# Performance work log

Measured on AMD Instinct MI355X. Metric: run time of the kernel, lower is better.

Reference implementation:

```python
import jax, jax.numpy as jnp
import numpy as np
import math

B, C, L, E, N = 16, 256, 2048, 512, 64
H = 2 * C  # S4 model dimension


def setup_inputs() -> dict:
    key = jax.random.key(0)
    ks = jax.random.split(key, 12)
    inp = {
        "x": jax.random.normal(ks[0], (B, C, L), dtype=jnp.float32),
        "diffusion_emb": jax.random.normal(ks[1], (B, E), dtype=jnp.float32),
        "dp_W": jax.random.normal(ks[2], (C, E), dtype=jnp.float32) / np.sqrt(E).astype(np.float32),
        "dp_b": jnp.zeros((C,), dtype=jnp.float32),
        "in_W": jax.random.normal(ks[3], (H, C), dtype=jnp.float32) / np.sqrt(C).astype(np.float32),
        "in_b": jnp.zeros((H,), dtype=jnp.float32),
        "out_W": jax.random.normal(ks[4], (2 * C, C), dtype=jnp.float32) / np.sqrt(C).astype(np.float32),
        "out_b": jnp.zeros((2 * C,), dtype=jnp.float32),
        "ln1_g": jnp.ones((H,), dtype=jnp.float32),
        "ln1_b": jnp.zeros((H,), dtype=jnp.float32),
        "ln2_g": jnp.ones((H,), dtype=jnp.float32),
        "ln2_b": jnp.zeros((H,), dtype=jnp.float32),
    }
    for i, pre in enumerate(["s41_", "s42_"]):
        k = jax.random.fold_in(key, 100 + i)
        k1, k2, k3, k4, k5 = jax.random.split(k, 5)
        # dt log-uniform in [1e-3, 1e-1] (standard S4 init)
        inp[pre + "log_dt"] = (jax.random.uniform(k1, (H,)) * (math.log(0.1) - math.log(0.001)) + math.log(0.001)).astype(jnp.float32)
        inp[pre + "A_re"] = (-0.5 * jnp.ones((H, N))).astype(jnp.float32)
        inp[pre + "A_im"] = jnp.tile(math.pi * jnp.arange(N, dtype=jnp.float32), (H, 1))
        inp[pre + "C_re"] = jax.random.normal(k2, (H, N), dtype=jnp.float32) * (0.5 ** 0.5)
        inp[pre + "C_im"] = jax.random.normal(k3, (H, N), dtype=jnp.float32) * (0.5 ** 0.5)
        inp[pre + "D"] = jax.random.normal(k4, (H,), dtype=jnp.float32)
        inp[pre + "oW"] = jax.random.normal(k5, (2 * H, H), dtype=jnp.float32) / np.sqrt(H).astype(np.float32)
        inp[pre + "ob"] = jnp.zeros((2 * H,), dtype=jnp.float32)
    return inp


def _s4(u, log_dt, A_re, A_im, C_re, C_im, D, oW, ob):
    # u: [B, H, L]. Diagonal SSM (S4D, ZOH discretization) -> FFT conv -> D skip -> GELU -> GLU output linear.
    Lq = u.shape[-1]
    dt = jnp.exp(log_dt)                       # [H]
    A = A_re + 1j * A_im                       # [H, N] diagonal state matrix
    Cc = C_re + 1j * C_im                      # [H, N]
    dtA = dt[:, None] * A                      # [H, N]
    Ct = Cc * (jnp.exp(dtA) - 1.0) / A         # ZOH-discretized C*B (B = 1)
    lr = jnp.arange(Lq)
    # Vandermonde kernel: K[h, l] = 2 Re sum_n Ct[h, n] exp(dtA[h, n] * l)
    K = 2.0 * jnp.real(jnp.einsum("hn,hnl->hl", Ct, jnp.exp(dtA[:, :, None] * lr)))  # [H, L]
    nfft = 2 * Lq
    y = jnp.fft.irfft(jnp.fft.rfft(u, n=nfft) * jnp.fft.rfft(K, n=nfft), n=nfft)[..., :Lq]
    y = y + D[None, :, None] * u
    y = jax.nn.gelu(y)
    y = jnp.einsum("oh,bhl->bol", oW, y) + ob[None, :, None]  # [B, 2H, L]
    a, b = jnp.split(y, 2, axis=1)             # GLU over channel dim
    return a * jax.nn.sigmoid(b)               # [B, H, L]


def _ln(y, g, b):
    # LayerNorm over the channel dim (module rearranges b c l -> b l c, LN(C), back)
    mu = jnp.mean(y, axis=1, keepdims=True)
    var = jnp.var(y, axis=1, keepdims=True)
    return (y - mu) * jax.lax.rsqrt(var + 1e-5) * g[None, :, None] + b[None, :, None]


def reference(x, diffusion_emb, dp_W, dp_b, in_W, in_b, out_W, out_b,
              ln1_g, ln1_b, ln2_g, ln2_b,
              s41_log_dt, s41_A_re, s41_A_im, s41_C_re, s41_C_im, s41_D, s41_oW, s41_ob,
              s42_log_dt, s42_A_re, s42_A_im, s42_C_re, s42_C_im, s42_D, s42_oW, s42_ob):
    d = diffusion_emb @ dp_W.T + dp_b          # [B, C] -> broadcast as [B, C, 1]
    y = x + d[:, :, None]
    y = jnp.einsum("oc,bcl->bol", in_W, y) + in_b[None, :, None]   # 1x1 conv: [B, 2C, L]
    y = _s4(y, s41_log_dt, s41_A_re, s41_A_im, s41_C_re, s41_C_im, s41_D, s41_oW, s41_ob)
    y = _ln(y, ln1_g, ln1_b)
    y = _s4(y, s42_log_dt, s42_A_re, s42_A_im, s42_C_re, s42_C_im, s42_D, s42_oW, s42_ob)
    y = _ln(y, ln2_g, ln2_b)
    gate, filt = jnp.split(y, 2, axis=1)
    y = jax.nn.sigmoid(gate) * jnp.tanh(filt)  # [B, C, L]
    y = jnp.einsum("oc,bcl->bol", out_W, y) + out_b[None, :, None]  # [B, 2C, L]
    residual, skip = jnp.split(y, 2, axis=1)
    return ((x + residual) / math.sqrt(2.0), skip)
```

## Files before the change

kernel.cpp:

```cpp
#include <hip/hip_runtime.h>
#include <math.h>

#define Bsz 16
#define Cch 256
#define Lsq 2048
#define Emb 512
#define Nst 64
#define Hch 512
#define KGP 2240

typedef _Float16 f16;
typedef _Float16 f16x8 __attribute__((ext_vector_type(8)));
typedef _Float16 f16x4 __attribute__((ext_vector_type(4)));
typedef float f32x4 __attribute__((ext_vector_type(4)));
typedef uint32_t u32x4 __attribute__((ext_vector_type(4)));

__device__ __forceinline__ float sigmoidf_(float x) { return 1.0f/(1.0f + __expf(-x)); }
__device__ __forceinline__ float gelu_tanh(float y) {
  float z = 0.7978845608028654f*(y + 0.044715f*y*y*y);
  float zc = fminf(fmaxf(z, -12.f), 12.f);
  float e = __expf(2.f*zc);
  return y - y/(e + 1.f);
}

__device__ __forceinline__ void gload_lds16(const f16* g, f16* l) {
  __builtin_amdgcn_global_load_lds(
      (const __attribute__((address_space(1))) void*)g,
      (__attribute__((address_space(3))) void*)l, 16, 0, 0);
}


__global__ void k_emb(const float* __restrict__ emb, const float* __restrict__ dpW,
                      const float* __restrict__ dpb, float* __restrict__ d) {
  int b = blockIdx.x, c = threadIdx.x;
  const float* e = emb + b*Emb;
  const float* w = dpW + c*Emb;
  float s = dpb[c];
  for (int k = 0; k < Emb; ++k) s += e[k]*w[k];
  d[b*Cch + c] = s;
}

__global__ void k_f2h4(const float* __restrict__ s1, f16* __restrict__ d1,
                       const float* __restrict__ s2, f16* __restrict__ d2,
                       const float* __restrict__ s3, f16* __restrict__ d3,
                       const float* __restrict__ s4, f16* __restrict__ d4) {
  int i = blockIdx.x*256 + threadIdx.x;
  const float* s; f16* d; int off;
  if (i < 32768)        { s = s1; d = d1; off = 0; }
  else if (i < 163840)  { s = s2; d = d2; off = 32768; }
  else if (i < 294912)  { s = s3; d = d3; off = 163840; }
  else                  { s = s4; d = d4; off = 294912; }
  int j = i - off;
  float4 v = ((const float4*)s)[j];
  f16x4 o;
  o[0] = (f16)v.x; o[1] = (f16)v.y; o[2] = (f16)v.z; o[3] = (f16)v.w;
  ((f16x4*)d)[j] = o;
}

__global__ void k_s4prep(const float* __restrict__ log_dt,
                         const float* __restrict__ A_re, const float* __restrict__ A_im,
                         const float* __restrict__ C_re, const float* __restrict__ C_im,
                         float* __restrict__ w_re, float* __restrict__ w_im,
                         float* __restrict__ ccr, float* __restrict__ cci) {
  int i = blockIdx.x*256 + threadIdx.x;
  if (i >= Hch*Nst) return;
  int h = i >> 6;
  float dt = expf(log_dt[h]);
  float Ar = A_re[i], Ai = A_im[i];
  float er = expf(dt*Ar);
  float wr = er*cosf(dt*Ai), wi = er*sinf(dt*Ai);
  float mag = Ar*Ar + Ai*Ai;
  float nr = wr - 1.0f, ni = wi;
  float qr = (nr*Ar + ni*Ai)/mag, qi = (ni*Ar - nr*Ai)/mag;
  float cr = C_re[i], ci = C_im[i];
  float tr = cr*qr - ci*qi, ti = cr*qi + ci*qr;
  w_re[i] = wr; w_im[i] = wi; ccr[i] = 2.0f*tr; cci[i] = -2.0f*ti;
}

__global__ __launch_bounds__(256) void k_kgen(
    const float* __restrict__ w_re, const float* __restrict__ w_im,
    const float* __restrict__ ccr, const float* __restrict__ cci,
    const float* __restrict__ Dvec,
    f16* __restrict__ Ke, f16* __restrict__ Ko) {
  __shared__ float2 wbt[64][65];
  __shared__ float2 wat[32][66];
  __shared__ float2 ccs[64];
  __shared__ float Kf[2048];
  int h = blockIdx.x, tid = threadIdx.x;
  if (tid < 64) {
    int n = tid;
    double wr = (double)w_re[h*64+n], wi = (double)w_im[h*64+n];
    double br = 1.0, bi = 0.0;
    for (int j = 0; j < 64; ++j) {
      wbt[n][j] = make_float2((float)br, (float)bi);
      double t = br*wr - bi*wi; bi = br*wi + bi*wr; br = t;
    }
    double ar = 1.0, ai = 0.0;
    for (int a = 0; a < 32; ++a) {
      wat[a][n] = make_float2((float)ar, (float)ai);
      double t = ar*br - ai*bi; ai = ar*bi + ai*br; ar = t;
    }
    ccs[n] = make_float2(ccr[h*64+n], cci[h*64+n]);
  }
  __syncthreads();
  int lane = tid & 63, wv = tid >> 6;
  float acc[8] = {0.f,0.f,0.f,0.f,0.f,0.f,0.f,0.f};
  for (int n = 0; n < 64; ++n) {
    float2 wb = wbt[n][lane];
    float2 cc = ccs[n];
    float tr = fmaf(cc.y, wb.y,  cc.x*wb.x);
    float ti = fmaf(cc.y, wb.x, -cc.x*wb.y);
    #pragma unroll
    for (int li = 0; li < 8; ++li) {
      float2 wa = wat[wv + 4*li][n];
      acc[li] = fmaf(wa.x, tr, acc[li]);
      acc[li] = fmaf(wa.y, ti, acc[li]);
    }
  }
  #pragma unroll
  for (int li = 0; li < 8; ++li)
    Kf[(wv + 4*li)*64 + lane] = acc[li];
  __syncthreads();
  if (tid == 0) Kf[0] += Dvec[h];
  __syncthreads();
  f16* keh = Ke + (size_t)h*KGP;
  f16* koh = Ko + (size_t)h*KGP;
  for (int q = tid; q < KGP; q += 256) {
    float e = (q < 2048) ? Kf[2047 - q] : 0.f;
    float o = (q < 2047) ? Kf[2046 - q] : 0.f;
    keh[q] = (f16)e; koh[q] = (f16)o;
  }
}

__device__ __forceinline__ f16x8 ld4u32(const uint32_t* __restrict__ p) {
  union { uint32_t u[4]; f16x8 v; } r;
  r.u[0] = p[0]; r.u[1] = p[1]; r.u[2] = p[2]; r.u[3] = p[3];
  return r.v;
}

__global__ __launch_bounds__(512) void k_conv(
    const f16* __restrict__ u, const f16* __restrict__ Ke, const f16* __restrict__ Ko,
    f16* __restrict__ g) {
  __shared__ __align__(16) f16 Ul[16*2048];
  int h = blockIdx.x, tid = threadIdx.x;
  {
    int b = tid >> 5, pr = tid & 31;
    const f16* src = u + ((size_t)b*Hch + h)*Lsq;
    f16* dst = &Ul[b*2048];
    #pragma unroll
    for (int c = 0; c < 8; ++c) {
      int gs = c*32 + pr;
      *(f16x8*)&dst[(gs ^ b)*8] = *(const f16x8*)(src + gs*8);
    }
  }
  __syncthreads();
  int wv = tid >> 6, lane = tid & 63;
  int m = lane & 15, qd = lane >> 4;
  const f16* keh = Ke + (size_t)h*KGP;
  const f16* koh = Ko + (size_t)h*KGP;
  const uint32_t* kb = (m & 1) ? (const uint32_t*)keh : (const uint32_t*)koh;
  f16* gb = g + ((size_t)m*Hch + h)*Lsq;
  const f16* ulb = &Ul[m*2048];
  for (int pi = 0; pi < 2; ++pi) {
    int P = pi ? (15 - wv) : wv;
    int i0 = P*128;
    int qb0 = 2047 - i0 - m + qd*8;
    int ib = qb0 >> 1;
    f32x4 acc[8];
    #pragma unroll
    for (int t = 0; t < 8; ++t) acc[t] = (f32x4){0.f,0.f,0.f,0.f};
    f16x8 W[8];
    #pragma unroll
    for (int t = 0; t < 8; ++t) W[t] = ld4u32(kb + ib - 8*t);
    int steps = 4*(P+1);
    for (int s4i = 0; s4i < steps; s4i += 4) {
      const uint32_t* pw = kb + ib + 16*(s4i + 1);
      #pragma unroll
      for (int ph = 0; ph < 4; ++ph) {
        int s = s4i + ph;
        f16x8 bf = *(const f16x8*)&ulb[((4*s + qd) ^ m)*8];
        f16x8 nf0 = ld4u32(pw + 16*ph);
        f16x8 nf1 = ld4u32(pw + 16*ph - 8);
        __builtin_amdgcn_s_setprio(1);
        #pragma unroll
        for (int t = 0; t < 8; ++t)
          acc[t] = __builtin_amdgcn_mfma_f32_16x16x32_f16(W[(t - 2*ph) & 7], bf, acc[t], 0, 0, 0);
        __builtin_amdgcn_s_setprio(0);
        W[(6 - 2*ph) & 7] = nf0;
        W[(7 - 2*ph) & 7] = nf1;
      }
    }
    #pragma unroll
    for (int t = 0; t < 8; ++t) {
      f16x4 o;
      #pragma unroll
      for (int r = 0; r < 4; ++r) o[r] = (f16)gelu_tanh(acc[t][r]);
      *(f16x4*)&gb[i0 + 16*t + qd*4] = o;
    }
  }
}

template<int KD, int MODE>
__global__ __launch_bounds__(512) void k_gemm(
    const f16* __restrict__ W, const f16* __restrict__ Bact,
    const float* __restrict__ bias, const float* __restrict__ xres,
    float* __restrict__ outF, f16* __restrict__ outH,
    const float* __restrict__ Bf32, const float* __restrict__ dadd) {
  constexpr int TOFF = (MODE == 1) ? 512 : 256;
  constexpr int NK = KD/32;
  constexpr int MT = (MODE == 1) ? 4 : 2;
  __shared__ __align__(16) f16 As[2][128*8*8];
  __shared__ __align__(16) uint32_t Bs[2][16*260];
  int tid = threadIdx.x;
  int wv = tid >> 6, lane = tid & 63;

  int nwg = 128*MT;
  int bid = blockIdx.x;
  int lin = (bid & 7)*(nwg >> 3) + (bid >> 3);
  int mt = lin % MT;
  int nt = lin / MT;
  int bb = nt >> 3;
  int l0 = (nt & 7)*256;
  int m0 = mt*128;
  int wm = (wv & 1)*64, wn = (wv >> 1)*64;
  int qd = lane >> 4, ln16 = lane & 15;

  f32x4 acc[2][4][4];
  #pragma unroll
  for (int t = 0; t < 2; ++t)
    for (int i = 0; i < 4; ++i)
      for (int j = 0; j < 4; ++j)
        acc[t][i][j] = (f32x4){0.f,0.f,0.f,0.f};

  const f16* Bbase = Bact + (size_t)bb*KD*Lsq + l0;
  const float* Bfb = Bf32 + (size_t)bb*KD*Lsq + l0;
  int q16 = tid >> 5, nch = tid & 31;

  auto stageA = [&](int buf, int kk) {
    #pragma unroll
    for (int i = 0; i < 2; ++i) {
      int gbase = (wv*2 + i)*64;
      int G = gbase + lane;
      int row = G >> 3;
      int gsw = (G & 7) ^ (row & 7);
      int t = gsw >> 2;
      const f16* src = W + (size_t)(m0 + row + t*TOFF)*KD + kk + (gsw & 3)*8;
      gload_lds16(src, &As[buf][gbase*8]);
    }
  };
  f16x8 rb0, rb1;
  float4 r0l, r0h, r1l, r1h;
  float d0, d1;
  auto loadB = [&](int kk) {
    if constexpr (MODE == 0) {
      const float* b0 = Bfb + (size_t)(kk + 2*q16)*Lsq + nch*8;
      r0l = *(const float4*)b0;      r0h = *(const float4*)(b0 + 4);
      r1l = *(const float4*)(b0 + Lsq); r1h = *(const float4*)(b0 + Lsq + 4);
      d0 = dadd[bb*Cch + kk + 2*q16];
      d1 = dadd[bb*Cch + kk + 2*q16 + 1];
    } else {
      const f16* b0 = Bbase + (size_t)(kk + 2*q16)*Lsq + nch*8;
      rb0 = *(const f16x8*)b0;
      rb1 = *(const f16x8*)(b0 + Lsq);
    }
  };
  auto packB = [&](int buf) {
    union { uint32_t w[8]; u32x4 v[2]; } pk;
    if constexpr (MODE == 0) {
      float a0[8] = {r0l.x,r0l.y,r0l.z,r0l.w,r0h.x,r0h.y,r0h.z,r0h.w};
      float a1[8] = {r1l.x,r1l.y,r1l.z,r1l.w,r1h.x,r1h.y,r1h.z,r1h.w};
      #pragma unroll
      for (int e = 0; e < 8; ++e) {
        union { f16 h2[2]; uint32_t u; } t2;
        t2.h2[0] = (f16)(a0[e] + d0); t2.h2[1] = (f16)(a1[e] + d1);
        pk.w[e] = t2.u;
      }
    } else {
      #pragma unroll
      for (int e = 0; e < 8; ++e) {
        union { f16 h2[2]; uint32_t u; } t2;
        t2.h2[0] = rb0[e]; t2.h2[1] = rb1[e];
        pk.w[e] = t2.u;
      }
    }
    *(u32x4*)&Bs[buf][q16*260 + nch*8]     = pk.v[0];
    *(u32x4*)&Bs[buf][q16*260 + nch*8 + 4] = pk.v[1];
  };
  auto compute = [&](int buf) {
    f16x8 afr[2][4];
    #pragma unroll
    for (int i = 0; i < 4; ++i)
      for (int t = 0; t < 2; ++t) {
        int row = wm + i*16 + ln16;
        int g = (t*4 + qd) ^ (row & 7);
        afr[t][i] = *(const f16x8*)&As[buf][(row*8 + g)*8];
      }
    f16x8 bfr[4];
    #pragma unroll
    for (int j = 0; j < 4; ++j) {
      union { uint32_t w2[4]; f16x8 v; } bu;
      #pragma unroll
      for (int r2 = 0; r2 < 4; ++r2) bu.w2[r2] = Bs[buf][(qd*4 + r2)*260 + wn + j*16 + ln16];
      bfr[j] = bu.v;
    }
    __builtin_amdgcn_s_setprio(1);
    #pragma unroll
    for (int j = 0; j < 4; ++j)
      for (int i = 0; i < 4; ++i)
        for (int t = 0; t < 2; ++t)
          acc[t][i][j] = __builtin_amdgcn_mfma_f32_16x16x32_f16(afr[t][i], bfr[j], acc[t][i][j], 0, 0, 0);
    __builtin_amdgcn_s_setprio(0);
  };

  stageA(0, 0);
  loadB(0);
  packB(0);
  __syncthreads();

  int cur = 0;
  for (int t = 0; t < NK; ++t) {
    if (t + 1 < NK) {
      stageA(cur ^ 1, (t + 1)*32);
      loadB((t + 1)*32);
    }
    compute(cur);
    if (t + 1 < NK) packB(cur ^ 1);
    __syncthreads();
    cur ^= 1;
  }

  #pragma unroll
  for (int i = 0; i < 4; ++i)
    for (int j = 0; j < 4; ++j)
      for (int r = 0; r < 4; ++r) {
        int ml = wm + i*16 + qd*4 + r;
        int nl = wn + j*16 + ln16;
        int mg = m0 + ml;
        int l  = l0 + nl;
        if (MODE == 0) {
          outH[((size_t)bb*Hch + mg)*Lsq + l]       = (f16)(acc[0][i][j][r] + bias[mg]);
          outH[((size_t)bb*Hch + mg + 256)*Lsq + l] = (f16)(acc[1][i][j][r] + bias[mg + 256]);
        } else if (MODE == 1) {
          float va = acc[0][i][j][r] + bias[mg];
          float vb = acc[1][i][j][r] + bias[512 + mg];
          outH[((size_t)bb*Hch + mg)*Lsq + l] = (f16)(va * sigmoidf_(vb));
        } else {
          size_t idx = ((size_t)bb*Cch + mg)*Lsq + l;
          float v0 = acc[0][i][j][r] + bias[mg];
          outF[idx] = (v0 + xres[idx]) * 0.7071067811865476f;
          float v1 = acc[1][i][j][r] + bias[mg + 256];
          outF[(size_t)Bsz*Cch*Lsq + idx] = v1;
        }
      }
}

template<int MODE>
__global__ __launch_bounds__(256) void k_ln(const f16* __restrict__ v,
                                            const float* __restrict__ gam, const float* __restrict__ bet,
                                            float* __restrict__ outF, f16* __restrict__ outH) {
  __shared__ float red[2][4][64];
  int b = blockIdx.x >> 5;
  int l = (blockIdx.x & 31)*64 + (threadIdx.x & 63);
  int wv = threadIdx.x >> 6, lane = threadIdx.x & 63;
  const f16* base = v + (size_t)b*Hch*Lsq + l;
  float s = 0.f, s2 = 0.f;
  for (int h = wv*128; h < wv*128 + 128; ++h) {
    float xv = (float)base[(size_t)h*Lsq];
    s += xv; s2 += xv*xv;
  }
  red[0][wv][lane] = s; red[1][wv][lane] = s2;
  __syncthreads();
  s  = red[0][0][lane] + red[0][1][lane] + red[0][2][lane] + red[0][3][lane];
  s2 = red[1][0][lane] + red[1][1][lane] + red[1][2][lane] + red[1][3][lane];
  float mu = s*(1.0f/Hch);
  float var = s2*(1.0f/Hch) - mu*mu;
  float rs = rsqrtf(var + 1e-5f);
  if (MODE == 0) {
    f16* ob = outH + (size_t)b*Hch*Lsq + l;
    for (int h = wv*128; h < wv*128 + 128; ++h)
      ob[(size_t)h*Lsq] = (f16)(((float)base[(size_t)h*Lsq] - mu)*rs*gam[h] + bet[h]);
  } else {
    f16* ob = outH + (size_t)b*Cch*Lsq + l;
    for (int c = wv*64; c < wv*64 + 64; ++c) {
      float xg = ((float)base[(size_t)c*Lsq] - mu)*rs*gam[c] + bet[c];
      float xf = ((float)base[(size_t)(c+Cch)*Lsq] - mu)*rs*gam[c+Cch] + bet[c+Cch];
      float xfc = fminf(fmaxf(xf, -15.f), 15.f);
      float e = __expf(2.f*xfc);
      ob[(size_t)c*Lsq] = (f16)(sigmoidf_(xg) * ((e-1.f)/(e+1.f)));
    }
  }
}

extern "C" void kernel_launch(void* const* d_in, const int* in_sizes, int n_in,
                              void* d_out, int out_size, void* d_ws, size_t ws_size,
                              hipStream_t stream) {
  const float* x    = (const float*)d_in[0];
  const float* emb  = (const float*)d_in[1];
  const float* dpW  = (const float*)d_in[2];
  const float* dpb  = (const float*)d_in[3];
  const float* inW  = (const float*)d_in[4];
  const float* inb  = (const float*)d_in[5];
  const float* outW = (const float*)d_in[6];
  const float* outb = (const float*)d_in[7];
  const float* ln1g = (const float*)d_in[8];
  const float* ln1b = (const float*)d_in[9];
  const float* ln2g = (const float*)d_in[10];
  const float* ln2b = (const float*)d_in[11];
  const float* s4[2][8];
  for (int ly = 0; ly < 2; ++ly)
    for (int k = 0; k < 8; ++k) s4[ly][k] = (const float*)d_in[12 + ly*8 + k];

  char* p = (char*)d_ws;
  auto alloc = [&](size_t bytes) { char* r = p; p += (bytes + 255) & ~(size_t)255; return r; };
  f16* inW16  = (f16*)alloc((size_t)Hch*Cch*2);
  f16* oW16_0 = (f16*)alloc((size_t)2*Hch*Hch*2);
  f16* oW16_1 = (f16*)alloc((size_t)2*Hch*Hch*2);
  f16* outW16 = (f16*)alloc((size_t)2*Cch*Cch*2);
  float* dbuf = (float*)alloc((size_t)Bsz*Cch*4);
  float* prm[2][4];
  for (int ly = 0; ly < 2; ++ly)
    for (int k = 0; k < 4; ++k) prm[ly][k] = (float*)alloc((size_t)Hch*Nst*4);
  f16* kge[2], *kgo[2];
  for (int ly = 0; ly < 2; ++ly) {
    kge[ly] = (f16*)alloc((size_t)Hch*KGP*2);
    kgo[ly] = (f16*)alloc((size_t)Hch*KGP*2);
  }
  f16*  xd   = (f16*)alloc((size_t)Bsz*Cch*Lsq*2);
  f16*  u16g = (f16*)alloc((size_t)Bsz*Hch*Lsq*2);
  f16*  gbuf = (f16*)alloc((size_t)Bsz*Hch*Lsq*2);
  f16*  glu  = (f16*)alloc((size_t)Bsz*Hch*Lsq*2);
  f16*  oW16[2] = {oW16_0, oW16_1};

  k_emb<<<Bsz, Cch, 0, stream>>>(emb, dpW, dpb, dbuf);
  k_f2h4<<<1280, 256, 0, stream>>>(inW, inW16, s4[0][6], oW16_0, s4[1][6], oW16_1, outW, outW16);
  for (int ly = 0; ly < 2; ++ly) {
    k_s4prep<<<(Hch*Nst+255)/256, 256, 0, stream>>>(s4[ly][0], s4[ly][1], s4[ly][2],
        s4[ly][3], s4[ly][4], prm[ly][0], prm[ly][1], prm[ly][2], prm[ly][3]);
    k_kgen<<<Hch, 256, 0, stream>>>(prm[ly][0], prm[ly][1], prm[ly][2], prm[ly][3],
        s4[ly][5], kge[ly], kgo[ly]);
  }

  dim3 bl(512);
  k_gemm<Cch, 0><<<256, bl, 0, stream>>>(inW16, nullptr, inb, nullptr, nullptr, u16g, x, dbuf);
  k_conv<<<Hch, 512, 0, stream>>>(u16g, kge[0], kgo[0], gbuf);
  k_gemm<Hch, 1><<<512, bl, 0, stream>>>(oW16[0], gbuf, s4[0][7], nullptr, nullptr, glu, nullptr, nullptr);
  k_ln<0><<<Bsz*32, 256, 0, stream>>>(glu, ln1g, ln1b, nullptr, u16g);
  k_conv<<<Hch, 512, 0, stream>>>(u16g, kge[1], kgo[1], gbuf);
  k_gemm<Hch, 1><<<512, bl, 0, stream>>>(oW16[1], gbuf, s4[1][7], nullptr, nullptr, glu, nullptr, nullptr);
  k_ln<1><<<Bsz*32, 256, 0, stream>>>(glu, ln2g, ln2b, nullptr, xd);
  k_gemm<Cch, 2><<<256, bl, 0, stream>>>(outW16, xd, outb, x, (float*)d_out, nullptr, nullptr, nullptr);
}
```

Baseline: 492.5 us.

## Fuse S4 param prep into kernel gen, batch both layers, parallelize emb GEMV

Folds the s4prep discretization into k_kgen so each block computes its own ZOH parameters, and launches kgen once for both S4 layers with a 1024-block grid. This removes three kernel launches and the intermediate parameter buffers. k_emb is rewritten to give one wavefront per (b,c) output, using float4 loads and a shuffle reduction instead of a serial 512-long loop per thread. The cost is a little redundant per-block work and a larger prologue in kgen.

After: 471.6 us. -4.2%, faster.

```diff
diff --git a/kernel.cpp b/kernel.cpp
--- a/kernel.cpp
+++ b/kernel.cpp
@@ -30,14 +30,22 @@
 }
 
 
-__global__ void k_emb(const float* __restrict__ emb, const float* __restrict__ dpW,
-                      const float* __restrict__ dpb, float* __restrict__ d) {
-  int b = blockIdx.x, c = threadIdx.x;
-  const float* e = emb + b*Emb;
-  const float* w = dpW + c*Emb;
-  float s = dpb[c];
-  for (int k = 0; k < Emb; ++k) s += e[k]*w[k];
-  d[b*Cch + c] = s;
+__global__ __launch_bounds__(256) void k_emb(const float* __restrict__ emb,
+                                             const float* __restrict__ dpW,
+                                             const float* __restrict__ dpb,
+                                             float* __restrict__ d) {
+  int wid = blockIdx.x*4 + (threadIdx.x >> 6);
+  int lane = threadIdx.x & 63;
+  int b = wid >> 8, c = wid & 255;
+  const float4* e4 = (const float4*)(emb + (size_t)b*Emb);
+  const float4* w4 = (const float4*)(dpW + (size_t)c*Emb);
+  float4 ev0 = e4[lane*2], ev1 = e4[lane*2 + 1];
+  float4 wv0 = w4[lane*2], wv1 = w4[lane*2 + 1];
+  float s = ev0.x*wv0.x + ev0.y*wv0.y + ev0.z*wv0.z + ev0.w*wv0.w
+          + ev1.x*wv1.x + ev1.y*wv1.y + ev1.z*wv1.z + ev1.w*wv1.w;
+  #pragma unroll
+  for (int off = 32; off; off >>= 1) s += __shfl_xor(s, off);
+  if (lane == 0) d[b*Cch + c] = dpb[c] + s;
 }
 
 __global__ void k_f2h4(const float* __restrict__ s1, f16* __restrict__ d1,
@@ -57,39 +65,40 @@
   ((f16x4*)d)[j] = o;
 }
 
-__global__ void k_s4prep(const float* __restrict__ log_dt,
-                         const float* __restrict__ A_re, const float* __restrict__ A_im,
-                         const float* __restrict__ C_re, const float* __restrict__ C_im,
-                         float* __restrict__ w_re, float* __restrict__ w_im,
-                         float* __restrict__ ccr, float* __restrict__ cci) {
-  int i = blockIdx.x*256 + threadIdx.x;
-  if (i >= Hch*Nst) return;
-  int h = i >> 6;
-  float dt = expf(log_dt[h]);
-  float Ar = A_re[i], Ai = A_im[i];
-  float er = expf(dt*Ar);
-  float wr = er*cosf(dt*Ai), wi = er*sinf(dt*Ai);
-  float mag = Ar*Ar + Ai*Ai;
-  float nr = wr - 1.0f, ni = wi;
-  float qr = (nr*Ar + ni*Ai)/mag, qi = (ni*Ar - nr*Ai)/mag;
-  float cr = C_re[i], ci = C_im[i];
-  float tr = cr*qr - ci*qi, ti = cr*qi + ci*qr;
-  w_re[i] = wr; w_im[i] = wi; ccr[i] = 2.0f*tr; cci[i] = -2.0f*ti;
-}
-
 __global__ __launch_bounds__(256) void k_kgen(
-    const float* __restrict__ w_re, const float* __restrict__ w_im,
-    const float* __restrict__ ccr, const float* __restrict__ cci,
-    const float* __restrict__ Dvec,
-    f16* __restrict__ Ke, f16* __restrict__ Ko) {
+    const float* __restrict__ ld0, const float* __restrict__ Ar0, const float* __restrict__ Ai0,
+    const float* __restrict__ Cr0, const float* __restrict__ Ci0, const float* __restrict__ D0,
+    const float* __restrict__ ld1, const float* __restrict__ Ar1, const float* __restrict__ Ai1,
+    const float* __restrict__ Cr1, const float* __restrict__ Ci1, const float* __restrict__ D1,
+    f16* __restrict__ Ke0, f16* __restrict__ Ko0,
+    f16* __restrict__ Ke1, f16* __restrict__ Ko1) {
   __shared__ float2 wbt[64][65];
   __shared__ float2 wat[32][66];
   __shared__ float2 ccs[64];
   __shared__ float Kf[2048];
-  int h = blockIdx.x, tid = threadIdx.x;
+  int h2 = blockIdx.x, tid = threadIdx.x;
+  int ly = h2 >> 9, h = h2 & 511;
+  const float* log_dt = ly ? ld1 : ld0;
+  const float* A_re = ly ? Ar1 : Ar0;
+  const float* A_im = ly ? Ai1 : Ai0;
+  const float* C_re = ly ? Cr1 : Cr0;
+  const float* C_im = ly ? Ci1 : Ci0;
+  const float* Dvec = ly ? D1 : D0;
+  f16* Ke = ly ? Ke1 : Ke0;
+  f16* Ko = ly ? Ko1 : Ko0;
   if (tid < 64) {
     int n = tid;
-    double wr = (double)w_re[h*64+n], wi = (double)w_im[h*64+n];
+    int i = h*64 + n;
+    float dt = expf(log_dt[h]);
+    float Arv = A_re[i], Aiv = A_im[i];
+    float er = expf(dt*Arv);
+    float wrf = er*cosf(dt*Aiv), wif = er*sinf(dt*Aiv);
+    float mag = Arv*Arv + Aiv*Aiv;
+    float nr = wrf - 1.0f, ni = wif;
+    float qr = (nr*Arv + ni*Aiv)/mag, qi = (ni*Arv - nr*Aiv)/mag;
+    float cr = C_re[i], ci = C_im[i];
+    float trc = cr*qr - ci*qi, tic = cr*qi + ci*qr;
+    double wr = (double)wrf, wi = (double)wif;
     double br = 1.0, bi = 0.0;
     for (int j = 0; j < 64; ++j) {
       wbt[n][j] = make_float2((float)br, (float)bi);
@@ -100,7 +109,7 @@
       wat[a][n] = make_float2((float)ar, (float)ai);
       double t = ar*br - ai*bi; ai = ar*bi + ai*br; ar = t;
     }
-    ccs[n] = make_float2(ccr[h*64+n], cci[h*64+n]);
+    ccs[n] = make_float2(2.0f*trc, -2.0f*tic);
   }
   __syncthreads();
   int lane = tid & 63, wv = tid >> 6;
@@ -417,9 +426,6 @@
   f16* oW16_1 = (f16*)alloc((size_t)2*Hch*Hch*2);
   f16* outW16 = (f16*)alloc((size_t)2*Cch*Cch*2);
   float* dbuf = (float*)alloc((size_t)Bsz*Cch*4);
-  float* prm[2][4];
-  for (int ly = 0; ly < 2; ++ly)
-    for (int k = 0; k < 4; ++k) prm[ly][k] = (float*)alloc((size_t)Hch*Nst*4);
   f16* kge[2], *kgo[2];
   for (int ly = 0; ly < 2; ++ly) {
     kge[ly] = (f16*)alloc((size_t)Hch*KGP*2);
@@ -431,14 +437,12 @@
   f16*  glu  = (f16*)alloc((size_t)Bsz*Hch*Lsq*2);
   f16*  oW16[2] = {oW16_0, oW16_1};
 
-  k_emb<<<Bsz, Cch, 0, stream>>>(emb, dpW, dpb, dbuf);
+  k_emb<<<1024, 256, 0, stream>>>(emb, dpW, dpb, dbuf);
   k_f2h4<<<1280, 256, 0, stream>>>(inW, inW16, s4[0][6], oW16_0, s4[1][6], oW16_1, outW, outW16);
-  for (int ly = 0; ly < 2; ++ly) {
-    k_s4prep<<<(Hch*Nst+255)/256, 256, 0, stream>>>(s4[ly][0], s4[ly][1], s4[ly][2],
-        s4[ly][3], s4[ly][4], prm[ly][0], prm[ly][1], prm[ly][2], prm[ly][3]);
-    k_kgen<<<Hch, 256, 0, stream>>>(prm[ly][0], prm[ly][1], prm[ly][2], prm[ly][3],
-        s4[ly][5], kge[ly], kgo[ly]);
-  }
+  k_kgen<<<1024, 256, 0, stream>>>(
+      s4[0][0], s4[0][1], s4[0][2], s4[0][3], s4[0][4], s4[0][5],
+      s4[1][0], s4[1][1], s4[1][2], s4[1][3], s4[1][4], s4[1][5],
+      kge[0], kgo[0], kge[1], kgo[1]);
 
   dim3 bl(512);
   k_gemm<Cch, 0><<<256, bl, 0, stream>>>(inW16, nullptr, inb, nullptr, nullptr, u16g, x, dbuf);
```
